# Kernel optimization log

Measured on AMD Instinct MI355X. Metric: run time of the kernel, lower is better.

## Reference

```python
import jax, jax.numpy as jnp
import numpy as np


def setup_inputs() -> dict:
    key = jax.random.key(0)
    ks = jax.random.split(key, 6)
    B = 65536
    x = jax.random.normal(ks[0], (B, 784), dtype=jnp.float32)
    conv_w = jax.random.normal(ks[1], (3, 3), dtype=jnp.float32)
    fc1_w = jax.random.normal(ks[2], (100, 676), dtype=jnp.float32) * (1.0 / np.sqrt(676))
    fc1_b = jax.random.normal(ks[3], (100,), dtype=jnp.float32) * 0.01
    fc2_w = jax.random.normal(ks[4], (10, 100), dtype=jnp.float32) * (1.0 / np.sqrt(100))
    fc2_b = jax.random.normal(ks[5], (10,), dtype=jnp.float32) * 0.01
    return {"x": x, "conv_w": conv_w, "fc1_w": fc1_w, "fc1_b": fc1_b, "fc2_w": fc2_w, "fc2_b": fc2_b}


def reference(x, conv_w, fc1_w, fc1_b, fc2_w, fc2_b):
    B = x.shape[0]
    img = x.reshape(B, 1, 28, 28)  # NCHW, single channel
    kern = conv_w.reshape(1, 1, 3, 3)  # OIHW
    # 'valid' cross-correlation, matching the slicing-based Convolve()
    conv = jax.lax.conv_general_dilated(
        img, kern, window_strides=(1, 1), padding='VALID',
        dimension_numbers=('NCHW', 'OIHW', 'NCHW'))  # [B,1,26,26]
    h = conv.reshape(B, 26 * 26)
    h = jax.nn.relu(h @ fc1_w.T + fc1_b)
    out = h @ fc2_w.T + fc2_b
    return out
```

## Files before the change

kernel.cpp:

```cpp
#include <hip/hip_runtime.h>


typedef short  s16x8 __attribute__((ext_vector_type(8)));
typedef float  f32x4 __attribute__((ext_vector_type(4)));

#define BM   64
#define HSTR 116
#define NT   8
#define NTL  7
#define KC   25

__device__ __forceinline__ unsigned short f2bf_rtne(float f) {
    unsigned int u = __builtin_bit_cast(unsigned int, f);
    u = (u + 0x7fffu + ((u >> 16) & 1u)) >> 16;
    return (unsigned short)u;
}

extern "C" __global__ void __launch_bounds__(256)
prep_w1eff(const float* __restrict__ W1, const float* __restrict__ cw9,
           const float* __restrict__ b1, unsigned short* __restrict__ bw)
{
    int id = blockIdx.x * 256 + threadIdx.x;
    if (id >= NT * KC * 64) return;
    int lane = id & 63;
    int kc   = (id >> 6) % KC;
    int t    = id / (KC * 64);
    int n    = t * 16 + (lane & 15);
    int k0   = kc * 32 + (lane >> 4) * 8;

    float cw[9];
#pragma unroll
    for (int i = 0; i < 9; ++i) cw[i] = cw9[i];

    unsigned short v[8];
#pragma unroll
    for (int j = 0; j < 8; ++j) {
        int k = k0 + j;
        float f = 0.f;
        if (n < 100) {
            if (k < 784) {
                int i = k / 28, jj = k % 28;
                for (int dr = 0; dr < 3; ++dr)
                    for (int dc = 0; dc < 3; ++dc) {
                        int a = i - dr, b = jj - dc;
                        if (a >= 0 && a < 26 && b >= 0 && b < 26)
                            f = fmaf(W1[(size_t)n * 676 + a * 26 + b],
                                     cw[dr * 3 + dc], f);
                    }
            } else if (k == 784) {
                f = b1[n];
            }
        }
        v[j] = f2bf_rtne(f);
    }
    *(uint4*)(bw + (size_t)id * 8) = *(const uint4*)v;
}

__device__ __forceinline__ s16x8 cvt8(float4 a, float4 b) {
    unsigned int ax = __builtin_bit_cast(unsigned int, a.x) + 0x8000u;
    unsigned int ay = __builtin_bit_cast(unsigned int, a.y) + 0x8000u;
    unsigned int az = __builtin_bit_cast(unsigned int, a.z) + 0x8000u;
    unsigned int aw = __builtin_bit_cast(unsigned int, a.w) + 0x8000u;
    unsigned int bx = __builtin_bit_cast(unsigned int, b.x) + 0x8000u;
    unsigned int by = __builtin_bit_cast(unsigned int, b.y) + 0x8000u;
    unsigned int bz = __builtin_bit_cast(unsigned int, b.z) + 0x8000u;
    unsigned int bw_ = __builtin_bit_cast(unsigned int, b.w) + 0x8000u;
    uint4 u;
    u.x = (ax >> 16) | (ay & 0xffff0000u);
    u.y = (az >> 16) | (aw & 0xffff0000u);
    u.z = (bx >> 16) | (by & 0xffff0000u);
    u.w = (bz >> 16) | (bw_ & 0xffff0000u);
    return __builtin_bit_cast(s16x8, u);
}

extern "C" __global__ void __launch_bounds__(256, 4)
digit_gemm(const float* __restrict__ x,
           const unsigned short* __restrict__ bw,
           const float* __restrict__ W2,
           const float* __restrict__ b2,
           float* __restrict__ out)
{
    __shared__ __align__(16) float hbuf[BM * HSTR];

    const int tid  = threadIdx.x;
    const int lane = tid & 63;
    const int wv   = tid >> 6;
    const int q    = lane >> 4;
    const int mn   = lane & 15;
    const int m0   = blockIdx.x * BM;

    const float* arow = x + (size_t)(m0 + wv * 16 + mn) * 784;
    const uint4* bwv  = (const uint4*)bw;

    f32x4 acc[NTL];
#pragma unroll
    for (int t = 0; t < NTL; ++t) {
        acc[t][0] = 0.f; acc[t][1] = 0.f; acc[t][2] = 0.f; acc[t][3] = 0.f;
    }

    float4 c0, c1;
    {
        const float* p = arow + q * 8;
        c0 = *(const float4*)p; c1 = *(const float4*)(p + 4);
    }

    for (int kc = 0; kc < KC; ++kc) {
        int kn  = (kc + 1 < KC) ? kc + 1 : KC - 1;
        int off = kn * 32 + q * 8;
        const float* p = arow + (off < 784 ? off : 0);
        float4 n0 = *(const float4*)p;
        float4 n1 = *(const float4*)(p + 4);

        uint4 bvv[NTL];
#pragma unroll
        for (int t = 0; t < NTL; ++t)
            bvv[t] = bwv[(size_t)(t * KC + kc) * 64 + lane];

        s16x8 av = cvt8(c0, c1);
        if (kc == KC - 1) {
            if (q >= 2) {
                uint4 z; z.x = (q == 2) ? 0x3F80u : 0u; z.y = 0u; z.z = 0u; z.w = 0u;
                av = __builtin_bit_cast(s16x8, z);
            }
        }

#pragma unroll
        for (int t = 0; t < NTL; ++t)
            acc[t] = __builtin_amdgcn_mfma_f32_16x16x32_bf16(
                av, __builtin_bit_cast(s16x8, bvv[t]), acc[t], 0, 0, 0);

        c0 = n0; c1 = n1;
    }

#pragma unroll
    for (int t = 0; t < NTL; ++t)
#pragma unroll
        for (int r = 0; r < 4; ++r) {
            float v = acc[t][r];
            v = v > 0.f ? v : 0.f;
            hbuf[(wv * 16 + q * 4 + r) * HSTR + t * 16 + mn] = v;
        }
    __syncthreads();

    for (int p = tid; p < BM * 10; p += 256) {
        int mi = p / 10, o = p - mi * 10;
        const float4* hv = (const float4*)(hbuf + mi * HSTR);
        const float4* w2 = (const float4*)(W2 + (size_t)o * 100);
        float s = b2[o];
#pragma unroll
        for (int g = 0; g < 25; ++g) {
            float4 h4 = hv[g], w4 = w2[g];
            s += h4.x * w4.x + h4.y * w4.y + h4.z * w4.z + h4.w * w4.w;
        }
        out[(size_t)(m0 + mi) * 10 + o] = s;
    }
}

extern "C" void kernel_launch(void* const* d_in, const int* in_sizes, int n_in,
                              void* d_out, int out_size, void* d_ws, size_t ws_size,
                              hipStream_t stream) {
    const float* x  = (const float*)d_in[0];
    const float* cw = (const float*)d_in[1];
    const float* W1 = (const float*)d_in[2];
    const float* b1 = (const float*)d_in[3];
    const float* W2 = (const float*)d_in[4];
    const float* b2 = (const float*)d_in[5];
    float* out = (float*)d_out;
    unsigned short* bw = (unsigned short*)d_ws;

    const int B = in_sizes[0] / 784;

    hipLaunchKernelGGL(prep_w1eff, dim3((NT * KC * 64 + 255) / 256), dim3(256),
                       0, stream, W1, cw, b1, bw);
    hipLaunchKernelGGL(digit_gemm, dim3(B / BM), dim3(256), 0, stream,
                       x, bw, W2, b2, out);
}
```

Before: 340.3 us.

## Make GEMM persistent with register-resident weights and double-buffered LDS x loads

Converts digit_gemm into a persistent kernel with 256 blocks, each looping over 16-row tiles. The bf16 effective weights are held in registers for the whole kernel, and W2 is staged once in LDS. Each next x tile is prefetched with global_load_lds into a double buffer while the current tile runs its MFMAs. This removes the repeated weight fetches from global memory and overlaps x streaming with compute. The costs are heavy register pressure (two 25-entry uint4 arrays per lane), one block per CU, and only 4 waves per CU to hide latency.

Result: faster. 319.1 us (-6.2%).

```diff
diff --git a/kernel.cpp b/kernel.cpp
--- a/kernel.cpp
+++ b/kernel.cpp
@@ -4,11 +4,14 @@
 typedef short  s16x8 __attribute__((ext_vector_type(8)));
 typedef float  f32x4 __attribute__((ext_vector_type(4)));
 
-#define BM   64
-#define HSTR 116
-#define NT   8
-#define NTL  7
-#define KC   25
+#define BM    16
+#define XP32  804
+#define HSTR  132
+#define NT    8
+#define KC    25
+#define GRID  256
+#define SLOTS (BM * 201)
+#define INSTS_PER_WAVE 13
 
 __device__ __forceinline__ unsigned short f2bf_rtne(float f) {
     unsigned int u = __builtin_bit_cast(unsigned int, f);
@@ -56,6 +59,14 @@
     *(uint4*)(bw + (size_t)id * 8) = *(const uint4*)v;
 }
 
+#define MFMA(a, b, c) __builtin_amdgcn_mfma_f32_16x16x32_bf16(a, b, c, 0, 0, 0)
+
+__device__ __forceinline__ void gld_lds16(const float* gsrc, float* ldst) {
+    __builtin_amdgcn_global_load_lds(
+        (const __attribute__((address_space(1))) unsigned int*)gsrc,
+        (__attribute__((address_space(3))) unsigned int*)ldst, 16, 0, 0);
+}
+
 __device__ __forceinline__ s16x8 cvt8(float4 a, float4 b) {
     unsigned int ax = __builtin_bit_cast(unsigned int, a.x) + 0x8000u;
     unsigned int ay = __builtin_bit_cast(unsigned int, a.y) + 0x8000u;
@@ -73,13 +84,16 @@
     return __builtin_bit_cast(s16x8, u);
 }
 
-extern "C" __global__ void __launch_bounds__(256, 4)
+extern "C" __global__ void __launch_bounds__(256, 1)
 digit_gemm(const float* __restrict__ x,
            const unsigned short* __restrict__ bw,
            const float* __restrict__ W2,
            const float* __restrict__ b2,
-           float* __restrict__ out)
+           float* __restrict__ out,
+           int ntiles)
 {
+    __shared__ __align__(16) float xbuf[2][BM * XP32];
+    __shared__ __align__(16) float w2buf[10 * 100];
     __shared__ __align__(16) float hbuf[BM * HSTR];
 
     const int tid  = threadIdx.x;
@@ -87,72 +101,102 @@
     const int wv   = tid >> 6;
     const int q    = lane >> 4;
     const int mn   = lane & 15;
-    const int m0   = blockIdx.x * BM;
-
-    const float* arow = x + (size_t)(m0 + wv * 16 + mn) * 784;
-    const uint4* bwv  = (const uint4*)bw;
-
-    f32x4 acc[NTL];
-#pragma unroll
-    for (int t = 0; t < NTL; ++t) {
-        acc[t][0] = 0.f; acc[t][1] = 0.f; acc[t][2] = 0.f; acc[t][3] = 0.f;
-    }
-
-    float4 c0, c1;
+    const int tile0 = blockIdx.x * ntiles;
+
+    const uint4* bwv = (const uint4*)bw;
+    const int t0 = wv, t1 = wv + 4;
+    uint4 br0[KC], br1[KC];
+#pragma unroll
+    for (int kc = 0; kc < KC; ++kc) {
+        br0[kc] = bwv[(t0 * KC + kc) * 64 + lane];
+        br1[kc] = bwv[(t1 * KC + kc) * 64 + lane];
+    }
+
+#pragma unroll
+    for (int i = 0; i < 4; ++i) {
+        int j = tid + 256 * i;
+        if (j < 1000) w2buf[j] = W2[j];
+    }
+    const bool has0 = (tid < BM * 10);
+    const int mi0 = tid / 10, o0 = tid - mi0 * 10;
+    const float bb0 = has0 ? b2[o0] : 0.f;
+
+    for (int s = tid; s < 2 * BM * 16; s += 256) {
+        int b = s >> 8, r = (s >> 4) & (BM - 1), d = s & 15;
+        xbuf[b][r * XP32 + 784 + d] = (d == 0) ? 1.0f : 0.f;
+    }
+
     {
-        const float* p = arow + q * 8;
-        c0 = *(const float4*)p; c1 = *(const float4*)(p + 4);
-    }
-
-    for (int kc = 0; kc < KC; ++kc) {
-        int kn  = (kc + 1 < KC) ? kc + 1 : KC - 1;
-        int off = kn * 32 + q * 8;
-        const float* p = arow + (off < 784 ? off : 0);
-        float4 n0 = *(const float4*)p;
-        float4 n1 = *(const float4*)(p + 4);
-
-        uint4 bvv[NTL];
-#pragma unroll
-        for (int t = 0; t < NTL; ++t)
-            bvv[t] = bwv[(size_t)(t * KC + kc) * 64 + lane];
-
-        s16x8 av = cvt8(c0, c1);
-        if (kc == KC - 1) {
-            if (q >= 2) {
-                uint4 z; z.x = (q == 2) ? 0x3F80u : 0u; z.y = 0u; z.z = 0u; z.w = 0u;
-                av = __builtin_bit_cast(s16x8, z);
-            }
-        }
-
-#pragma unroll
-        for (int t = 0; t < NTL; ++t)
-            acc[t] = __builtin_amdgcn_mfma_f32_16x16x32_bf16(
-                av, __builtin_bit_cast(s16x8, bvv[t]), acc[t], 0, 0, 0);
-
-        c0 = n0; c1 = n1;
-    }
-
-#pragma unroll
-    for (int t = 0; t < NTL; ++t)
+        const float* xg = x + (size_t)tile0 * BM * 784;
+#pragma unroll
+        for (int i = 0; i < INSTS_PER_WAVE; ++i) {
+            int sb   = (wv * INSTS_PER_WAVE + i) * 64;
+            int slot = sb + lane;
+            int m    = slot / 201, c4 = slot - m * 201;
+            if (slot < SLOTS && c4 < 196)
+                gld_lds16(xg + (size_t)m * 784 + c4 * 4, &xbuf[0][sb * 4]);
+        }
+    }
+    asm volatile("s_waitcnt vmcnt(0)" ::: "memory");
+    __syncthreads();
+
+    for (int t = 0; t < ntiles; ++t) {
+        const int cur = t & 1;
+        const int m0  = (tile0 + t) * BM;
+
+        if (t + 1 < ntiles) {
+            const float* xg = x + (size_t)(tile0 + t + 1) * BM * 784;
+#pragma unroll
+            for (int i = 0; i < INSTS_PER_WAVE; ++i) {
+                int sb   = (wv * INSTS_PER_WAVE + i) * 64;
+                int slot = sb + lane;
+                int m    = slot / 201, c4 = slot - m * 201;
+                if (slot < SLOTS && c4 < 196)
+                    gld_lds16(xg + (size_t)m * 784 + c4 * 4,
+                              &xbuf[cur ^ 1][sb * 4]);
+            }
+        }
+
+        f32x4 acc0, acc1;
+#pragma unroll
+        for (int i = 0; i < 4; ++i) { acc0[i] = 0.f; acc1[i] = 0.f; }
+        const float* ar = &xbuf[cur][mn * XP32 + q * 8];
+#pragma unroll
+        for (int kc = 0; kc < KC; ++kc) {
+            float4 f0 = *(const float4*)(ar + kc * 32);
+            float4 f1 = *(const float4*)(ar + kc * 32 + 4);
+            s16x8 av = cvt8(f0, f1);
+            acc0 = MFMA(av, __builtin_bit_cast(s16x8, br0[kc]), acc0);
+            if (wv < 3)
+                acc1 = MFMA(av, __builtin_bit_cast(s16x8, br1[kc]), acc1);
+        }
+
 #pragma unroll
         for (int r = 0; r < 4; ++r) {
-            float v = acc[t][r];
-            v = v > 0.f ? v : 0.f;
-            hbuf[(wv * 16 + q * 4 + r) * HSTR + t * 16 + mn] = v;
-        }
-    __syncthreads();
-
-    for (int p = tid; p < BM * 10; p += 256) {
-        int mi = p / 10, o = p - mi * 10;
-        const float4* hv = (const float4*)(hbuf + mi * HSTR);
-        const float4* w2 = (const float4*)(W2 + (size_t)o * 100);
-        float s = b2[o];
-#pragma unroll
-        for (int g = 0; g < 25; ++g) {
-            float4 h4 = hv[g], w4 = w2[g];
-            s += h4.x * w4.x + h4.y * w4.y + h4.z * w4.z + h4.w * w4.w;
-        }
-        out[(size_t)(m0 + mi) * 10 + o] = s;
+            int row = q * 4 + r;
+            float z;
+            z = acc0[r]; z = z > 0.f ? z : 0.f; hbuf[row * HSTR + t0 * 16 + mn] = z;
+            if (wv < 3) {
+                z = acc1[r]; z = z > 0.f ? z : 0.f; hbuf[row * HSTR + t1 * 16 + mn] = z;
+            }
+        }
+        asm volatile("s_waitcnt lgkmcnt(0)" ::: "memory");
+        __builtin_amdgcn_s_barrier();
+
+        if (has0) {
+            const float4* hv = (const float4*)(hbuf + mi0 * HSTR);
+            const float4* w2 = (const float4*)(w2buf + o0 * 100);
+            float s = bb0;
+#pragma unroll
+            for (int g = 0; g < 25; ++g) {
+                float4 h4 = hv[g], w4 = w2[g];
+                s += h4.x * w4.x + h4.y * w4.y + h4.z * w4.z + h4.w * w4.w;
+            }
+            out[(size_t)(m0 + mi0) * 10 + o0] = s;
+        }
+
+        asm volatile("s_waitcnt vmcnt(0)" ::: "memory");
+        __builtin_amdgcn_s_barrier();
     }
 }
 
@@ -169,9 +213,10 @@
     unsigned short* bw = (unsigned short*)d_ws;
 
     const int B = in_sizes[0] / 784;
+    const int ntiles = (B / BM) / GRID;
 
     hipLaunchKernelGGL(prep_w1eff, dim3((NT * KC * 64 + 255) / 256), dim3(256),
                        0, stream, W1, cw, b1, bw);
-    hipLaunchKernelGGL(digit_gemm, dim3(B / BM), dim3(256), 0, stream,
-                       x, bw, W2, b2, out);
-}
+    hipLaunchKernelGGL(digit_gemm, dim3(GRID), dim3(256), 0, stream,
+                       x, bw, W2, b2, out, ntiles);
+}
```
